# Performance work log

Hardware: AMD Instinct MI355X
Metric: run time of the kernel (lower is better)

## Reference

```python
import jax, jax.numpy as jnp
import numpy as np

B, C, H, W, NH = 2, 192, 256, 256, 4


def setup_inputs() -> dict:
    key = jax.random.key(0)
    k0, k1, k2, k3 = jax.random.split(key, 4)
    x = jax.random.normal(k0, (B, C, H, W), jnp.float32)
    qkv_w = jax.random.normal(k1, (3 * C, C), jnp.float32) * 0.02      # 1x1 conv as matmul
    dw_w = jax.random.normal(k2, (3 * C, 1, 3, 3), jnp.float32) * 0.02  # depthwise 3x3, groups=3C
    proj_w = jax.random.normal(k3, (C, C), jnp.float32) * 0.02          # 1x1 output conv
    temperature = jnp.ones((NH, 1, 1), jnp.float32)
    return dict(x=x, qkv_w=qkv_w, dw_w=dw_w, proj_w=proj_w, temperature=temperature)


def reference(x, qkv_w, dw_w, proj_w, temperature):
    b, c, hgt, wid = x.shape
    nh = temperature.shape[0]
    hd = c // nh  # head channel dim

    # 1x1 pointwise qkv projection (Conv2d(C, 3C, 1, bias=False))
    qkv = jnp.einsum('bchw,oc->bohw', x, qkv_w)
    # 3x3 depthwise conv, groups = 3C, padding=1
    qkv = jax.lax.conv_general_dilated(
        qkv, dw_w, window_strides=(1, 1), padding='SAME',
        dimension_numbers=('NCHW', 'OIHW', 'NCHW'),
        feature_group_count=3 * c)

    q, k, v = jnp.split(qkv, 3, axis=1)
    # b (h c) x y -> b h c (x y)
    q = q.reshape(b, nh, hd, hgt * wid)
    k = k.reshape(b, nh, hd, hgt * wid)
    v = v.reshape(b, nh, hd, hgt * wid)

    # F.normalize(dim=-1): L2 normalize over spatial axis, eps clamp like torch
    eps = 1e-12
    q = q / jnp.maximum(jnp.linalg.norm(q, axis=-1, keepdims=True), eps)
    k = k / jnp.maximum(jnp.linalg.norm(k, axis=-1, keepdims=True), eps)

    # CxC channel attention per head, scaled by learned temperature
    attn = jnp.einsum('bhcn,bhdn->bhcd', q, k) * temperature  # [b, nh, hd, hd]
    attn = jax.nn.softmax(attn, axis=-1)
    out = jnp.einsum('bhcd,bhdn->bhcn', attn, v)

    # b h c (x y) -> b (h c) x y
    out = out.reshape(b, c, hgt, wid)
    # 1x1 output projection
    return jnp.einsum('bchw,oc->bohw', out, proj_w)
```

## Files before the change

### kernel.cpp

```cpp
#include <hip/hip_runtime.h>

typedef __attribute__((ext_vector_type(8))) short short8;
typedef __attribute__((ext_vector_type(4))) float f32x4;
typedef __attribute__((ext_vector_type(4))) unsigned short u16x4;

#define B_   2
#define C_   192
#define NH_  4
#define HD_  48
#define CO_  576
#define HGT_ 256
#define WID_ 256
#define NSP_ 65536

__device__ __forceinline__ unsigned short f2bf(float f) {
  unsigned int u = __float_as_uint(f);
  u += 0x7FFFu + ((u >> 16) & 1u);
  return (unsigned short)(u >> 16);
}
__device__ __forceinline__ float bf2f(unsigned short h) {
  return __uint_as_float(((unsigned int)h) << 16);
}
__device__ __forceinline__ int swz(int n) { return (n & 7) ^ ((n >> 3) & 7); }

__global__ void k_cvtA(const float* __restrict__ src, unsigned short* __restrict__ dst) {
  int i = blockIdx.x * 256 + threadIdx.x;
  if (i >= CO_ * C_) return;
  int m = i / C_, k = i % C_;
  int f = m >> 4, l15 = m & 15, kk = k >> 5, lg = (k >> 3) & 3, j = k & 7;
  dst[((((f * 6 + kk) * 4 + lg) * 16 + l15) << 3) + j] = f2bf(src[i]);
}

template<int MBLOCKS, int TPB, bool X_BF16, bool OUT_BF16>
__global__ __launch_bounds__(256, 2)
void k_gemm(const unsigned short* __restrict__ Aperm, long aBatchStride,
            const void* __restrict__ Xin, long xBatchStride, int xChanOff,
            void* __restrict__ Out, long outBatchStride)
{
  constexpr int NSETX = 1024 / TPB / 8;
  __shared__ unsigned short Xs[192 * 72];
  const int tid = threadIdx.x;
  const int b = blockIdx.z;
  int mb, nset;
  {
    int orig = blockIdx.x;
    int xcd = orig & 7, wid = orig >> 3;
    if (MBLOCKS == 3) { mb = wid % 3; nset = xcd * NSETX + wid / 3; }
    else              { mb = 0;       nset = xcd * NSETX + wid; }
  }

  const int sn = tid & 15, sk = tid >> 4;
  const int n0 = sn * 4, hh = sk & 1;
  const float* Xf = (const float*)Xin + (size_t)b * xBatchStride + (size_t)xChanOff * NSP_;
  const unsigned short* Xh = (const unsigned short*)Xin + (size_t)b * xBatchStride + (size_t)xChanOff * NSP_;

  const int wave = tid >> 6, lane = tid & 63;
  const int l15 = lane & 15, lg = lane >> 4;
  const int fragM0 = mb * 12 + wave * 3;
  const unsigned short* Ap = Aperm + (size_t)b * aBatchStride;

  short8 af[6][3];
#pragma unroll
  for (int kk = 0; kk < 6; kk++)
#pragma unroll
    for (int fm = 0; fm < 3; fm++)
      af[kk][fm] = *(const short8*)(Ap + (((size_t)((fragM0 + fm) * 6 + kk) * 64 + lane) << 3));

  f32x4 rf[3][4];
  u16x4 rh[3][4];
  auto LOADT = [&](int nb) {
    const size_t cb = (size_t)nb * 64 + n0;
#pragma unroll
    for (int it = 0; it < 3; it++) {
      if (!X_BF16) {
        const float* p = Xf + (size_t)(it * 64 + sk * 4) * NSP_ + cb;
#pragma unroll
        for (int r = 0; r < 4; r++) rf[it][r] = *(const f32x4*)(p + (size_t)r * NSP_);
      } else {
        const unsigned short* p = Xh + (size_t)(it * 64 + sk * 4) * NSP_ + cb;
#pragma unroll
        for (int r = 0; r < 4; r++) rh[it][r] = *(const u16x4*)(p + (size_t)r * NSP_);
      }
    }
  };
  auto WRITEC = [&]() {
#pragma unroll
    for (int it = 0; it < 3; it++) {
      const int u16v = it * 8 + (sk >> 1);
#pragma unroll
      for (int j = 0; j < 4; j++) {
        int n = n0 + j;
        u16x4 w;
        if (!X_BF16) { w[0] = f2bf(rf[it][0][j]); w[1] = f2bf(rf[it][1][j]);
                       w[2] = f2bf(rf[it][2][j]); w[3] = f2bf(rf[it][3][j]); }
        else         { w[0] = rh[it][0][j]; w[1] = rh[it][1][j];
                       w[2] = rh[it][2][j]; w[3] = rh[it][3][j]; }
        *(u16x4*)&Xs[n * 192 + ((u16v ^ swz(n)) << 3) + (hh << 2)] = w;
      }
    }
  };

  LOADT(nset * TPB);
  for (int t = 0; t < TPB; t++) {
    const int nb = nset * TPB + t;
    WRITEC();
    asm volatile("s_waitcnt lgkmcnt(0)" ::: "memory");
    __builtin_amdgcn_s_barrier();
    if (t + 1 < TPB) LOADT(nb + 1);

    f32x4 acc[3][4];
#pragma unroll
    for (int i = 0; i < 3; i++)
#pragma unroll
      for (int j = 0; j < 4; j++) acc[i][j] = (f32x4){0.f, 0.f, 0.f, 0.f};

#pragma unroll
    for (int kk = 0; kk < 6; kk++) {
      const int ur = kk * 4 + lg;
      short8 bfr[4];
#pragma unroll
      for (int fn = 0; fn < 4; fn++) {
        int col = fn * 16 + l15;
        bfr[fn] = *(const short8*)(&Xs[col * 192 + ((ur ^ swz(col)) << 3)]);
      }
      __builtin_amdgcn_s_setprio(1);
#pragma unroll
      for (int fm = 0; fm < 3; fm++)
#pragma unroll
        for (int fn = 0; fn < 4; fn++)
          acc[fm][fn] = __builtin_amdgcn_mfma_f32_16x16x32_bf16(bfr[fn], af[kk][fm], acc[fm][fn], 0, 0, 0);
      __builtin_amdgcn_s_setprio(0);
    }

    if (OUT_BF16) {
      asm volatile("s_waitcnt lgkmcnt(0)" ::: "memory");
      __builtin_amdgcn_s_barrier();
#pragma unroll
      for (int fm = 0; fm < 3; fm++) {
        int mloc = (wave * 3 + fm) * 16 + l15;
#pragma unroll
        for (int fn = 0; fn < 4; fn++) {
          u16x4 w;
          w[0] = f2bf(acc[fm][fn][0]); w[1] = f2bf(acc[fm][fn][1]);
          w[2] = f2bf(acc[fm][fn][2]); w[3] = f2bf(acc[fm][fn][3]);
          *(u16x4*)&Xs[mloc * 72 + fn * 16 + lg * 4] = w;
        }
      }
      asm volatile("s_waitcnt lgkmcnt(0)" ::: "memory");
      __builtin_amdgcn_s_barrier();
      unsigned short* O = (unsigned short*)Out + (size_t)b * outBatchStride +
                          (size_t)mb * 192 * NSP_ + (size_t)nb * 64;
#pragma unroll
      for (int i = 0; i < 6; i++) {
        int p = tid + i * 256, row = p >> 3, cB = (p & 7) * 8;
        short8 v = *(const short8*)&Xs[row * 72 + cB];
        *(short8*)(O + (size_t)row * NSP_ + cB) = v;
      }
      asm volatile("s_waitcnt lgkmcnt(0)" ::: "memory");
      __builtin_amdgcn_s_barrier();
    } else {
      float* O = (float*)Out + (size_t)b * outBatchStride;
      const size_t ncol0 = (size_t)nb * 64;
#pragma unroll
      for (int fm = 0; fm < 3; fm++) {
        int m = (fragM0 + fm) * 16 + l15;
#pragma unroll
        for (int fn = 0; fn < 4; fn++)
          *(f32x4*)(O + (size_t)m * NSP_ + ncol0 + fn * 16 + lg * 4) = acc[fm][fn];
      }
      asm volatile("s_waitcnt lgkmcnt(0)" ::: "memory");
      __builtin_amdgcn_s_barrier();
    }
  }
}

#define DW_RB 32
__global__ __launch_bounds__(256, 6)
void k_dw(const unsigned short* __restrict__ qkv, const float* __restrict__ dww,
          unsigned short* __restrict__ out, float* __restrict__ sumsq)
{
  __shared__ unsigned short rows[34][272];
  const int ch = blockIdx.y;
  const int b  = blockIdx.z;
  const int tid = threadIdx.x;
  const int ybase = blockIdx.x * DW_RB;

  const unsigned short* in = qkv + ((size_t)b * CO_ + ch) * NSP_;
  unsigned short* o = out + ((size_t)b * CO_ + ch) * NSP_;
  float w[9];
#pragma unroll
  for (int i = 0; i < 9; i++) w[i] = dww[ch * 9 + i];

  short8 st[5];
#pragma unroll
  for (int i = 0; i < 5; i++) {
    int u = tid + i * 256;
    if (u < 1088) {
      int r = u >> 5, sg = u & 31;
      int yy = ybase - 1 + r;
      short8 z = {0, 0, 0, 0, 0, 0, 0, 0};
      if ((unsigned)yy < (unsigned)HGT_) z = *(const short8*)(in + (size_t)yy * WID_ + sg * 8);
      st[i] = z;
    }
  }
#pragma unroll
  for (int i = 0; i < 5; i++) {
    int u = tid + i * 256;
    if (u < 1088) {
      int r = u >> 5, sg = u & 31;
      *(short8*)&rows[r][8 + sg * 8] = st[i];
    }
  }
  if (tid < 68) rows[tid >> 1][(tid & 1) ? 264 : 7] = 0;
  __syncthreads();

  const int seg = tid & 31, rowblk = tid >> 5;
  const int c0 = 8 + seg * 8;
  float win[3][10];
  float ss = 0.f;
#pragma unroll
  for (int i = 0; i < 6; i++) {
    const int lr = rowblk * 4 + i;
    float* f = win[i % 3];
    short8 v = *(const short8*)&rows[lr][c0];
#pragma unroll
    for (int j = 0; j < 8; j++) f[j + 1] = bf2f((unsigned short)v[j]);
    f[0] = bf2f(rows[lr][c0 - 1]);
    f[9] = bf2f(rows[lr][c0 + 8]);
    if (i >= 2) {
      const float* a  = win[(i - 2) % 3];
      const float* bb = win[(i - 1) % 3];
      const float* cc = f;
      short8 ov;
#pragma unroll
      for (int j = 0; j < 8; j++) {
        float acc = a[j]  * w[0] + a[j + 1]  * w[1] + a[j + 2]  * w[2]
                  + bb[j] * w[3] + bb[j + 1] * w[4] + bb[j + 2] * w[5]
                  + cc[j] * w[6] + cc[j + 1] * w[7] + cc[j + 2] * w[8];
        ov[j] = (short)f2bf(acc);
        ss += acc * acc;
      }
      *(short8*)(o + (size_t)(ybase + rowblk * 4 + i - 2) * WID_ + seg * 8) = ov;
    }
  }

  if (ch < 2 * C_) {
#pragma unroll
    for (int off = 32; off > 0; off >>= 1) ss += __shfl_down(ss, off);
    __shared__ float wsum[4];
    if ((tid & 63) == 0) wsum[tid >> 6] = ss;
    __syncthreads();
    if (tid == 0) atomicAdd(&sumsq[b * 2 * C_ + ch], wsum[0] + wsum[1] + wsum[2] + wsum[3]);
  }
}

__global__ __launch_bounds__(256)
void k_qk(const unsigned short* __restrict__ qkvd, float* __restrict__ part)
{
  const int chunk = blockIdx.x;
  const int h = blockIdx.y, b = blockIdx.z;
  const int tid = threadIdx.x;
  const int wave = tid >> 6, lane = tid & 63;
  const int l15 = lane & 15, lg = lane >> 4;
  const unsigned short* qb = qkvd + (size_t)b * CO_ * NSP_ + (size_t)(h * HD_) * NSP_;
  const unsigned short* kb = qkvd + (size_t)b * CO_ * NSP_ + (size_t)(C_ + h * HD_) * NSP_;
  const int kbase = chunk * 1024 + wave * 256;

  f32x4 acc[3][3];
#pragma unroll
  for (int i = 0; i < 3; i++)
#pragma unroll
    for (int j = 0; j < 3; j++) acc[i][j] = (f32x4){0.f, 0.f, 0.f, 0.f};

#pragma unroll
  for (int ks = 0; ks < 8; ks++) {
    const int k0 = kbase + ks * 32 + lg * 8;
    short8 af[3], bfr[3];
#pragma unroll
    for (int i = 0; i < 3; i++)
      af[i] = *(const short8*)(qb + (size_t)(i * 16 + l15) * NSP_ + k0);
#pragma unroll
    for (int i = 0; i < 3; i++)
      bfr[i] = *(const short8*)(kb + (size_t)(i * 16 + l15) * NSP_ + k0);
#pragma unroll
    for (int fm = 0; fm < 3; fm++)
#pragma unroll
      for (int fn = 0; fn < 3; fn++)
        acc[fm][fn] = __builtin_amdgcn_mfma_f32_16x16x32_bf16(af[fm], bfr[fn], acc[fm][fn], 0, 0, 0);
  }

  __shared__ float red[4][HD_ * HD_];
#pragma unroll
  for (int fm = 0; fm < 3; fm++)
#pragma unroll
    for (int fn = 0; fn < 3; fn++)
#pragma unroll
      for (int r = 0; r < 4; r++)
        red[wave][(fm * 16 + lg * 4 + r) * HD_ + fn * 16 + l15] = acc[fm][fn][r];
  __syncthreads();

  float* P = part + ((size_t)(b * NH_ + h) * 64 + chunk) * (HD_ * HD_);
#pragma unroll
  for (int j = 0; j < 9; j++) {
    int e = tid + j * 256;
    P[e] = red[0][e] + red[1][e] + red[2][e] + red[3][e];
  }
}

__global__ __launch_bounds__(256)
void k_smax(const float* __restrict__ part, const float* __restrict__ sumsq,
            const float* __restrict__ temp, const float* __restrict__ projw,
            unsigned short* __restrict__ M)
{
  const int h = blockIdx.x, b = blockIdx.y;
  const int tid = threadIdx.x;
  __shared__ float lgt[HD_][HD_];
  __shared__ float at[HD_][HD_];
  __shared__ float pw[C_][HD_];
  const float tmp = temp[h];
  const float* P = part + (size_t)(b * NH_ + h) * 64 * (HD_ * HD_);

  float s[9];
#pragma unroll
  for (int j = 0; j < 9; j++) s[j] = 0.f;
  for (int p = 0; p < 64; p++) {
    const float* Pp = P + (size_t)p * (HD_ * HD_);
#pragma unroll
    for (int j = 0; j < 9; j++) s[j] += Pp[tid + j * 256];
  }
#pragma unroll
  for (int j = 0; j < 9; j++) {
    int e = tid + j * 256;
    int c = e / HD_, d = e % HD_;
    float nq = fmaxf(sqrtf(sumsq[b * 2 * C_ + h * HD_ + c]), 1e-12f);
    float nk = fmaxf(sqrtf(sumsq[b * 2 * C_ + C_ + h * HD_ + d]), 1e-12f);
    lgt[c][d] = s[j] / (nq * nk) * tmp;
  }
  for (int e = tid; e < C_ * HD_; e += 256) {
    int o = e / HD_, c = e % HD_;
    pw[o][c] = projw[o * C_ + h * HD_ + c];
  }
  __syncthreads();
  if (tid < HD_) {
    float mx = -1e30f;
    for (int d = 0; d < HD_; d++) mx = fmaxf(mx, lgt[tid][d]);
    float ssum = 0.f;
    for (int d = 0; d < HD_; d++) { float e_ = expf(lgt[tid][d] - mx); at[tid][d] = e_; ssum += e_; }
    float inv = 1.f / ssum;
    for (int d = 0; d < HD_; d++) at[tid][d] *= inv;
  }
  __syncthreads();
  unsigned short* Mo = M + (size_t)b * C_ * C_;
  for (int e = tid; e < C_ * HD_; e += 256) {
    int o = e / HD_, d = e % HD_;
    float sm = 0.f;
    for (int c = 0; c < HD_; c++) sm += pw[o][c] * at[c][d];
    int col = h * HD_ + d;
    int f = o >> 4, l15 = o & 15, kk = col >> 5, lg = (col >> 3) & 3, j = col & 7;
    Mo[((((f * 6 + kk) * 4 + lg) * 16 + l15) << 3) + j] = f2bf(sm);
  }
}

extern "C" void kernel_launch(void* const* d_in, const int* in_sizes, int n_in,
                              void* d_out, int out_size, void* d_ws, size_t ws_size,
                              hipStream_t stream)
{
  const float* x     = (const float*)d_in[0];
  const float* qkvw  = (const float*)d_in[1];
  const float* dww   = (const float*)d_in[2];
  const float* projw = (const float*)d_in[3];
  const float* temp  = (const float*)d_in[4];
  float* out         = (float*)d_out;

  char* ws = (char*)d_ws;
  size_t off = 0;
  auto alloc = [&](size_t bytes) { void* p = ws + off; off += (bytes + 255) & ~(size_t)255; return p; };
  unsigned short* qkvd_bf = (unsigned short*)alloc((size_t)B_ * CO_ * NSP_ * 2);
  unsigned short* qkv_bf  = (unsigned short*)alloc((size_t)B_ * CO_ * NSP_ * 2);
  unsigned short* qkvw_bf = (unsigned short*)alloc((size_t)CO_ * C_ * 2);
  unsigned short* M_bf    = (unsigned short*)alloc((size_t)B_ * C_ * C_ * 2);
  float* sumsq            = (float*)alloc((size_t)B_ * 2 * C_ * 4);
  float* part             = (float*)alloc((size_t)B_ * NH_ * 64 * HD_ * HD_ * 4);

  hipMemsetAsync(sumsq, 0, (size_t)B_ * 2 * C_ * 4, stream);
  k_cvtA<<<dim3((CO_ * C_ + 255) / 256), dim3(256), 0, stream>>>(qkvw, qkvw_bf);
  k_gemm<3, 8, false, true><<<dim3(384, 1, B_), dim3(256), 0, stream>>>(
      qkvw_bf, 0, x, (long)C_ * NSP_, 0, qkv_bf, (long)CO_ * NSP_);
  k_dw<<<dim3(HGT_ / DW_RB, CO_, B_), dim3(256), 0, stream>>>(qkv_bf, dww, qkvd_bf, sumsq);
  k_qk<<<dim3(64, NH_, B_), dim3(256), 0, stream>>>(qkvd_bf, part);
  k_smax<<<dim3(NH_, B_), dim3(256), 0, stream>>>(part, sumsq, temp, projw, M_bf);
  k_gemm<1, 4, true, false><<<dim3(256, 1, B_), dim3(256), 0, stream>>>(
      M_bf, (long)C_ * C_, qkvd_bf, (long)CO_ * NSP_, 2 * C_, out, (long)C_ * NSP_);
}
```

Before: 224.2 us.

## Transpose V to spatial-major and use register-resident M GEMM for output

Adds a transpose kernel that rewrites the V channels into an [n][C] bf16 layout, and a new final GEMM kernel that keeps the whole per-wave slice of M in registers and reads V fragments directly from global memory, with no shared-memory staging. The existing k_gemm launch bound is also raised to 3 blocks per SM. The aim is to drop the LDS staging and sync overhead of the final projection GEMM. The price is an extra full read and write of V (about 50 MB of traffic) plus another kernel launch, and higher register pressure under the tighter launch bound.

```diff
diff --git a/kernel.cpp b/kernel.cpp
--- a/kernel.cpp
+++ b/kernel.cpp
@@ -32,7 +32,7 @@
 }
 
 template<int MBLOCKS, int TPB, bool X_BF16, bool OUT_BF16>
-__global__ __launch_bounds__(256, 2)
+__global__ __launch_bounds__(256, 3)
 void k_gemm(const unsigned short* __restrict__ Aperm, long aBatchStride,
             const void* __restrict__ Xin, long xBatchStride, int xChanOff,
             void* __restrict__ Out, long outBatchStride)
@@ -251,6 +251,32 @@
     if ((tid & 63) == 0) wsum[tid >> 6] = ss;
     __syncthreads();
     if (tid == 0) atomicAdd(&sumsq[b * 2 * C_ + ch], wsum[0] + wsum[1] + wsum[2] + wsum[3]);
+  }
+}
+
+__global__ __launch_bounds__(256)
+void k_cvtV(const unsigned short* __restrict__ qkvd, unsigned short* __restrict__ vT)
+{
+  __shared__ unsigned short t[64][264];
+  const int n0 = blockIdx.x * 256, dv0 = blockIdx.y * 64, b = blockIdx.z;
+  const int tid = threadIdx.x;
+  const unsigned short* src = qkvd + ((size_t)b * CO_ + 2 * C_ + dv0) * NSP_ + n0;
+  const int r = tid >> 5, c8 = (tid & 31) * 8;
+#pragma unroll
+  for (int i = 0; i < 8; i++) {
+    int dv = i * 8 + r;
+    *(short8*)&t[dv][c8] = *(const short8*)(src + (size_t)dv * NSP_ + c8);
+  }
+  __syncthreads();
+  unsigned short* dst = vT + ((size_t)b * NSP_ + n0) * C_ + dv0;
+  const int nr = tid >> 3, dc = (tid & 7) * 8;
+#pragma unroll
+  for (int i = 0; i < 8; i++) {
+    int n = i * 32 + nr;
+    short8 v;
+#pragma unroll
+    for (int j = 0; j < 8; j++) v[j] = (short)t[dc + j][n];
+    *(short8*)(dst + (size_t)n * C_ + dc) = v;
   }
 }
 
@@ -361,6 +387,62 @@
   }
 }
 
+template<int TPB>
+__global__ __launch_bounds__(256, 3)
+void k_mv(const unsigned short* __restrict__ Mperm, const unsigned short* __restrict__ vT,
+          float* __restrict__ out)
+{
+  const int tid = threadIdx.x;
+  const int b = blockIdx.z;
+  const int nset = blockIdx.x;
+  const int wave = tid >> 6, lane = tid & 63;
+  const int l15 = lane & 15, lg = lane >> 4;
+  const int fragM0 = wave * 3;
+  const unsigned short* Mp = Mperm + (size_t)b * C_ * C_;
+  const unsigned short* V = vT + (size_t)b * NSP_ * C_;
+  float* O = out + (size_t)b * C_ * NSP_;
+
+  short8 af[6][3];
+#pragma unroll
+  for (int kk = 0; kk < 6; kk++)
+#pragma unroll
+    for (int fm = 0; fm < 3; fm++)
+      af[kk][fm] = *(const short8*)(Mp + (((size_t)((fragM0 + fm) * 6 + kk) * 64 + lane) << 3));
+
+  for (int t = 0; t < TPB; t++) {
+    const int nb = nset * TPB + t;
+    f32x4 acc[3][4];
+#pragma unroll
+    for (int i = 0; i < 3; i++)
+#pragma unroll
+      for (int j = 0; j < 4; j++) acc[i][j] = (f32x4){0.f, 0.f, 0.f, 0.f};
+
+#pragma unroll
+    for (int kk = 0; kk < 6; kk++) {
+      short8 bfr[4];
+#pragma unroll
+      for (int fn = 0; fn < 4; fn++) {
+        int n = nb * 64 + fn * 16 + l15;
+        bfr[fn] = *(const short8*)(V + (size_t)n * C_ + kk * 32 + lg * 8);
+      }
+#pragma unroll
+      for (int fm = 0; fm < 3; fm++)
+#pragma unroll
+        for (int fn = 0; fn < 4; fn++)
+          acc[fm][fn] = __builtin_amdgcn_mfma_f32_16x16x32_bf16(bfr[fn], af[kk][fm], acc[fm][fn], 0, 0, 0);
+    }
+
+    const size_t ncol0 = (size_t)nb * 64;
+#pragma unroll
+    for (int fm = 0; fm < 3; fm++) {
+      int m = (fragM0 + fm) * 16 + l15;
+#pragma unroll
+      for (int fn = 0; fn < 4; fn++)
+        *(f32x4*)(O + (size_t)m * NSP_ + ncol0 + fn * 16 + lg * 4) = acc[fm][fn];
+    }
+  }
+}
+
 extern "C" void kernel_launch(void* const* d_in, const int* in_sizes, int n_in,
                               void* d_out, int out_size, void* d_ws, size_t ws_size,
                               hipStream_t stream)
@@ -377,6 +459,7 @@
   auto alloc = [&](size_t bytes) { void* p = ws + off; off += (bytes + 255) & ~(size_t)255; return p; };
   unsigned short* qkvd_bf = (unsigned short*)alloc((size_t)B_ * CO_ * NSP_ * 2);
   unsigned short* qkv_bf  = (unsigned short*)alloc((size_t)B_ * CO_ * NSP_ * 2);
+  unsigned short* vT_bf   = (unsigned short*)alloc((size_t)B_ * NSP_ * C_ * 2);
   unsigned short* qkvw_bf = (unsigned short*)alloc((size_t)CO_ * C_ * 2);
   unsigned short* M_bf    = (unsigned short*)alloc((size_t)B_ * C_ * C_ * 2);
   float* sumsq            = (float*)alloc((size_t)B_ * 2 * C_ * 4);
@@ -387,8 +470,8 @@
   k_gemm<3, 8, false, true><<<dim3(384, 1, B_), dim3(256), 0, stream>>>(
       qkvw_bf, 0, x, (long)C_ * NSP_, 0, qkv_bf, (long)CO_ * NSP_);
   k_dw<<<dim3(HGT_ / DW_RB, CO_, B_), dim3(256), 0, stream>>>(qkv_bf, dww, qkvd_bf, sumsq);
+  k_cvtV<<<dim3(NSP_ / 256, C_ / 64, B_), dim3(256), 0, stream>>>(qkvd_bf, vT_bf);
   k_qk<<<dim3(64, NH_, B_), dim3(256), 0, stream>>>(qkvd_bf, part);
   k_smax<<<dim3(NH_, B_), dim3(256), 0, stream>>>(part, sumsq, temp, projw, M_bf);
-  k_gemm<1, 4, true, false><<<dim3(256, 1, B_), dim3(256), 0, stream>>>(
-      M_bf, (long)C_ * C_, qkvd_bf, (long)CO_ * NSP_, 2 * C_, out, (long)C_ * NSP_);
-}
+  k_mv<4><<<dim3(256, 1, B_), dim3(256), 0, stream>>>(M_bf, vT_bf, out);
+}
```

Measured after the change: 343.7 us. 53.3% more time.

## Use 12-wave blocks covering all 576 qkv rows so each X tile is loaded once

Applied to the files above, without the earlier changes.

The qkv GEMM previously split the 576 output rows across three 256-thread blocks, each reloading and converting the same X tile. It now uses one 768-thread block (12 waves) per column set, so the tile is staged once in shared memory and feeds all output rows. The bf16 epilogue now writes directly to global memory instead of staging through LDS, which removes two barriers but produces narrower 8-byte stores. The projection GEMM launch also changes to twice as many blocks with fewer tiles per block, and the larger blocks change register pressure and occupancy.

```diff
diff --git a/kernel.cpp b/kernel.cpp
--- a/kernel.cpp
+++ b/kernel.cpp
@@ -31,32 +31,34 @@
   dst[((((f * 6 + kk) * 4 + lg) * 16 + l15) << 3) + j] = f2bf(src[i]);
 }
 
-template<int MBLOCKS, int TPB, bool X_BF16, bool OUT_BF16>
-__global__ __launch_bounds__(256, 2)
+template<int NWAVES, int TPB, bool X_BF16, bool OUT_BF16>
+__global__ __launch_bounds__(NWAVES * 64, NWAVES == 12 ? 3 : 2)
 void k_gemm(const unsigned short* __restrict__ Aperm, long aBatchStride,
             const void* __restrict__ Xin, long xBatchStride, int xChanOff,
             void* __restrict__ Out, long outBatchStride)
 {
-  constexpr int NSETX = 1024 / TPB / 8;
-  __shared__ unsigned short Xs[192 * 72];
+  constexpr int T = NWAVES * 64;
+  constexpr int S = 12288 / (16 * T);
+  constexpr int KG = T >> 4;
+  constexpr int NSETX = (1024 / TPB) / 8;
+  __shared__ unsigned short Xs[64 * 192];
   const int tid = threadIdx.x;
   const int b = blockIdx.z;
-  int mb, nset;
+  int nset;
   {
     int orig = blockIdx.x;
     int xcd = orig & 7, wid = orig >> 3;
-    if (MBLOCKS == 3) { mb = wid % 3; nset = xcd * NSETX + wid / 3; }
-    else              { mb = 0;       nset = xcd * NSETX + wid; }
+    nset = xcd * NSETX + wid;
   }
 
   const int sn = tid & 15, sk = tid >> 4;
-  const int n0 = sn * 4, hh = sk & 1;
+  const int n0 = sn * 4;
   const float* Xf = (const float*)Xin + (size_t)b * xBatchStride + (size_t)xChanOff * NSP_;
   const unsigned short* Xh = (const unsigned short*)Xin + (size_t)b * xBatchStride + (size_t)xChanOff * NSP_;
 
   const int wave = tid >> 6, lane = tid & 63;
   const int l15 = lane & 15, lg = lane >> 4;
-  const int fragM0 = mb * 12 + wave * 3;
+  const int fragM0 = wave * 3;
   const unsigned short* Ap = Aperm + (size_t)b * aBatchStride;
 
   short8 af[6][3];
@@ -66,18 +68,19 @@
     for (int fm = 0; fm < 3; fm++)
       af[kk][fm] = *(const short8*)(Ap + (((size_t)((fragM0 + fm) * 6 + kk) * 64 + lane) << 3));
 
-  f32x4 rf[3][4];
-  u16x4 rh[3][4];
+  f32x4 rf[S][4];
+  u16x4 rh[S][4];
   auto LOADT = [&](int nb) {
     const size_t cb = (size_t)nb * 64 + n0;
 #pragma unroll
-    for (int it = 0; it < 3; it++) {
+    for (int it = 0; it < S; it++) {
+      const int krow = (it * KG + sk) * 4;
       if (!X_BF16) {
-        const float* p = Xf + (size_t)(it * 64 + sk * 4) * NSP_ + cb;
+        const float* p = Xf + (size_t)krow * NSP_ + cb;
 #pragma unroll
         for (int r = 0; r < 4; r++) rf[it][r] = *(const f32x4*)(p + (size_t)r * NSP_);
       } else {
-        const unsigned short* p = Xh + (size_t)(it * 64 + sk * 4) * NSP_ + cb;
+        const unsigned short* p = Xh + (size_t)krow * NSP_ + cb;
 #pragma unroll
         for (int r = 0; r < 4; r++) rh[it][r] = *(const u16x4*)(p + (size_t)r * NSP_);
       }
@@ -85,8 +88,9 @@
   };
   auto WRITEC = [&]() {
 #pragma unroll
-    for (int it = 0; it < 3; it++) {
-      const int u16v = it * 8 + (sk >> 1);
+    for (int it = 0; it < S; it++) {
+      const int g = it * KG + sk;
+      const int u16v = g >> 1, hh = g & 1;
 #pragma unroll
       for (int j = 0; j < 4; j++) {
         int n = n0 + j;
@@ -132,35 +136,22 @@
       __builtin_amdgcn_s_setprio(0);
     }
 
+    const size_t ncol0 = (size_t)nb * 64;
     if (OUT_BF16) {
-      asm volatile("s_waitcnt lgkmcnt(0)" ::: "memory");
-      __builtin_amdgcn_s_barrier();
+      unsigned short* O = (unsigned short*)Out + (size_t)b * outBatchStride;
 #pragma unroll
       for (int fm = 0; fm < 3; fm++) {
-        int mloc = (wave * 3 + fm) * 16 + l15;
+        int m = (fragM0 + fm) * 16 + l15;
 #pragma unroll
         for (int fn = 0; fn < 4; fn++) {
           u16x4 w;
           w[0] = f2bf(acc[fm][fn][0]); w[1] = f2bf(acc[fm][fn][1]);
           w[2] = f2bf(acc[fm][fn][2]); w[3] = f2bf(acc[fm][fn][3]);
-          *(u16x4*)&Xs[mloc * 72 + fn * 16 + lg * 4] = w;
+          *(u16x4*)(O + (size_t)m * NSP_ + ncol0 + fn * 16 + lg * 4) = w;
         }
       }
-      asm volatile("s_waitcnt lgkmcnt(0)" ::: "memory");
-      __builtin_amdgcn_s_barrier();
-      unsigned short* O = (unsigned short*)Out + (size_t)b * outBatchStride +
-                          (size_t)mb * 192 * NSP_ + (size_t)nb * 64;
-#pragma unroll
-      for (int i = 0; i < 6; i++) {
-        int p = tid + i * 256, row = p >> 3, cB = (p & 7) * 8;
-        short8 v = *(const short8*)&Xs[row * 72 + cB];
-        *(short8*)(O + (size_t)row * NSP_ + cB) = v;
-      }
-      asm volatile("s_waitcnt lgkmcnt(0)" ::: "memory");
-      __builtin_amdgcn_s_barrier();
     } else {
       float* O = (float*)Out + (size_t)b * outBatchStride;
-      const size_t ncol0 = (size_t)nb * 64;
 #pragma unroll
       for (int fm = 0; fm < 3; fm++) {
         int m = (fragM0 + fm) * 16 + l15;
@@ -168,9 +159,10 @@
         for (int fn = 0; fn < 4; fn++)
           *(f32x4*)(O + (size_t)m * NSP_ + ncol0 + fn * 16 + lg * 4) = acc[fm][fn];
       }
-      asm volatile("s_waitcnt lgkmcnt(0)" ::: "memory");
-      __builtin_amdgcn_s_barrier();
-    }
+    }
+
+    asm volatile("s_waitcnt lgkmcnt(0)" ::: "memory");
+    __builtin_amdgcn_s_barrier();
   }
 }
 
@@ -384,11 +376,11 @@
 
   hipMemsetAsync(sumsq, 0, (size_t)B_ * 2 * C_ * 4, stream);
   k_cvtA<<<dim3((CO_ * C_ + 255) / 256), dim3(256), 0, stream>>>(qkvw, qkvw_bf);
-  k_gemm<3, 8, false, true><<<dim3(384, 1, B_), dim3(256), 0, stream>>>(
+  k_gemm<12, 8, false, true><<<dim3(128, 1, B_), dim3(768), 0, stream>>>(
       qkvw_bf, 0, x, (long)C_ * NSP_, 0, qkv_bf, (long)CO_ * NSP_);
   k_dw<<<dim3(HGT_ / DW_RB, CO_, B_), dim3(256), 0, stream>>>(qkv_bf, dww, qkvd_bf, sumsq);
   k_qk<<<dim3(64, NH_, B_), dim3(256), 0, stream>>>(qkvd_bf, part);
   k_smax<<<dim3(NH_, B_), dim3(256), 0, stream>>>(part, sumsq, temp, projw, M_bf);
-  k_gemm<1, 4, true, false><<<dim3(256, 1, B_), dim3(256), 0, stream>>>(
+  k_gemm<4, 2, true, false><<<dim3(512, 1, B_), dim3(256), 0, stream>>>(
       M_bf, (long)C_ * C_, qkvd_bf, (long)CO_ * NSP_, 2 * C_, out, (long)C_ * NSP_);
 }
```

After: 300.3 us. +34.0%, slower.
